# Kernel optimization log

Hardware: AMD Instinct MI355X
Metric: run time of the kernel (lower is better)

The kernel has to match this reference:

```python
import jax, jax.numpy as jnp
import numpy as np

EPS_NORM = 1e-8  # F.normalize eps (clamps norm from below)
EPS_ERR = 1e-8   # eps added under sqrt for the error


def _normalize(x, eps=EPS_NORM):
    n = jnp.linalg.norm(x, axis=-1, keepdims=True)
    return x / jnp.maximum(n, eps)


def _frame_basis(frames):
    """frames: [b, n, 3, 3]; points a, b, c are the COLUMNS (unbind dim=-1).
    Returns origin b_pt [b, n, 3] and orthonormal basis E [b, n, 3(basis k), 3(xyz d)]."""
    a, b_pt, c = frames[..., 0], frames[..., 1], frames[..., 2]
    w1 = _normalize(a - b_pt)
    w2 = _normalize(c - b_pt)
    e1 = _normalize(w1 + w2)
    e2 = _normalize(w2 - w1)
    e3 = jnp.cross(e1, e2)
    return b_pt, jnp.stack([e1, e2, e3], axis=-2)


def _pair_transform(coords, frames):
    """t[b,i,j,k] = dot(coords[b,i] - origin[b,j], E[b,j,k]).
    Exploits linearity to avoid materializing the [b,n,n,3] difference tensor."""
    origin, E = _frame_basis(frames)
    proj_c = jnp.einsum('bid,bjkd->bijk', coords, E)          # [b,n,n,3]
    proj_o = jnp.einsum('bjd,bjkd->bjk', origin, E)           # [b,n,3]
    return proj_c - proj_o[:, None, :, :]


def setup_inputs() -> dict:
    key = jax.random.key(0)
    k1, k2, k3, k4 = jax.random.split(key, 4)
    b, n = 2, 2048
    return {
        'pred_coords': jax.random.normal(k1, (b, n, 3), dtype=jnp.float32),
        'true_coords': jax.random.normal(k2, (b, n, 3), dtype=jnp.float32),
        'pred_frames': jax.random.normal(k3, (b, n, 3, 3), dtype=jnp.float32),
        'true_frames': jax.random.normal(k4, (b, n, 3, 3), dtype=jnp.float32),
    }


def reference(pred_coords, true_coords, pred_frames, true_frames):
    # coord index i is expressed in frame index j -> errors [b, n, n]
    t_pred = _pair_transform(pred_coords, pred_frames)
    t_true = _pair_transform(true_coords, true_frames)
    diff = t_pred - t_true
    return jnp.sqrt(jnp.sum(diff * diff, axis=-1) + EPS_ERR)
```

## Files before the change

kernel.cpp:

```cpp
#include <hip/hip_runtime.h>
#include <math.h>

#define EPS_NORM 1e-8f
#define EPS_ERR  1e-8f

__device__ inline void norm3(float& x, float& y, float& z) {
    float nn = sqrtf(x*x + y*y + z*z);
    float inv = 1.0f / fmaxf(nn, EPS_NORM);
    x *= inv; y *= inv; z *= inv;
}

__device__ inline void basis_from_frame(const float* __restrict__ F, size_t base,
                                        float* e , float* o ) {
    float ax = F[base + 0], bx = F[base + 1], cx = F[base + 2];
    float ay = F[base + 3], by = F[base + 4], cy = F[base + 5];
    float az = F[base + 6], bz = F[base + 7], cz = F[base + 8];
    float w1x = ax - bx, w1y = ay - by, w1z = az - bz;
    float w2x = cx - bx, w2y = cy - by, w2z = cz - bz;
    norm3(w1x, w1y, w1z);
    norm3(w2x, w2y, w2z);
    float e1x = w1x + w2x, e1y = w1y + w2y, e1z = w1z + w2z;
    float e2x = w2x - w1x, e2y = w2y - w1y, e2z = w2z - w1z;
    norm3(e1x, e1y, e1z);
    norm3(e2x, e2y, e2z);
    float e3x = e1y * e2z - e1z * e2y;
    float e3y = e1z * e2x - e1x * e2z;
    float e3z = e1x * e2y - e1y * e2x;
    e[0] = e1x; e[1] = e1y; e[2] = e1z;
    e[3] = e2x; e[4] = e2y; e[5] = e2z;
    e[6] = e3x; e[7] = e3y; e[8] = e3z;
    o[0] = bx * e1x + by * e1y + bz * e1z;
    o[1] = bx * e2x + by * e2y + bz * e2z;
    o[2] = bx * e3x + by * e3y + bz * e3z;
}

__global__ __launch_bounds__(256) void frames_kernel(
    const float* __restrict__ predF, const float* __restrict__ trueF,
    float* __restrict__ fd, int total_bn)
{
    int idx = blockIdx.x * 256 + threadIdx.x;
    if (idx >= total_bn) return;
    float ep[9], op[3], et[9], ot[3];
    basis_from_frame(predF, (size_t)idx * 9, ep, op);
    basis_from_frame(trueF, (size_t)idx * 9, et, ot);
    #pragma unroll
    for (int k = 0; k < 9; ++k) fd[(size_t)k * total_bn + idx] = ep[k];
    #pragma unroll
    for (int k = 0; k < 9; ++k) fd[(size_t)(9 + k) * total_bn + idx] = et[k];
    #pragma unroll
    for (int k = 0; k < 3; ++k) fd[(size_t)(18 + k) * total_bn + idx] = op[k] - ot[k];
}

template<int IT>
__global__ __launch_bounds__(256) void pair_err_kernel(
    const float* __restrict__ cp, const float* __restrict__ ct,
    const float* __restrict__ fd, float* __restrict__ out, int n, int total_bn)
{
    int j  = blockIdx.x * 256 + threadIdx.x;
    int bi = blockIdx.z;
    if (j >= n) return;
    int idx = bi * n + j;

    float f[21];
    #pragma unroll
    for (int c = 0; c < 21; ++c) f[c] = fd[(size_t)c * total_bn + idx];

    const int i0 = blockIdx.y * IT;
    const int iters = min(IT, n - i0);
    size_t obase = ((size_t)bi * n + i0) * n + j;
    size_t cbase = ((size_t)bi * n + i0) * 3;

    #pragma unroll 8
    for (int ii = 0; ii < iters; ++ii) {
        float px = cp[cbase + ii * 3 + 0], py = cp[cbase + ii * 3 + 1], pz = cp[cbase + ii * 3 + 2];
        float tx = ct[cbase + ii * 3 + 0], ty = ct[cbase + ii * 3 + 1], tz = ct[cbase + ii * 3 + 2];
        float d0 = px * f[0] + py * f[1] + pz * f[2] - (tx * f[ 9] + ty * f[10] + tz * f[11]) - f[18];
        float d1 = px * f[3] + py * f[4] + pz * f[5] - (tx * f[12] + ty * f[13] + tz * f[14]) - f[19];
        float d2 = px * f[6] + py * f[7] + pz * f[8] - (tx * f[15] + ty * f[16] + tz * f[17]) - f[20];
        out[obase + (size_t)ii * n] = sqrtf(d0 * d0 + d1 * d1 + d2 * d2 + EPS_ERR);
    }
}

extern "C" void kernel_launch(void* const* d_in, const int* in_sizes, int n_in,
                              void* d_out, int out_size, void* d_ws, size_t ws_size,
                              hipStream_t stream) {
    const float* pred_coords = (const float*)d_in[0];
    const float* true_coords = (const float*)d_in[1];
    const float* pred_frames = (const float*)d_in[2];
    const float* true_frames = (const float*)d_in[3];
    float* out = (float*)d_out;

    int total_bn = in_sizes[0] / 3;
    int n = (int)((long long)out_size / total_bn);
    int b = total_bn / n;

    float* fd = (float*)d_ws;

    int blocks1 = (total_bn + 255) / 256;
    frames_kernel<<<blocks1, 256, 0, stream>>>(pred_frames, true_frames, fd, total_bn);

    constexpr int IT = 32;
    dim3 grid((n + 255) / 256, (n + IT - 1) / IT, b);
    pair_err_kernel<IT><<<grid, 256, 0, stream>>>(pred_coords, true_coords, fd, out, n, total_bn);
}
```

Measured before the change: 84.08 us.

## Fuse frame basis computation into pair kernel and store two columns per thread

Drops the separate frames kernel and its workspace round-trip. Each pair-error block now recomputes the orthonormal bases for its own j columns straight from the raw frame inputs. Each thread handles two adjacent j columns and writes them as a float2 store, halving the coordinate loads per output. The cost is redundant basis recomputation in every i-tile block (n/32 times per frame), more registers, and uncoalesced 9-float frame loads.

```diff
diff --git a/kernel.cpp b/kernel.cpp
--- a/kernel.cpp
+++ b/kernel.cpp
@@ -34,50 +34,84 @@
     o[2] = bx * e3x + by * e3y + bz * e3z;
 }
 
-__global__ __launch_bounds__(256) void frames_kernel(
-    const float* __restrict__ predF, const float* __restrict__ trueF,
-    float* __restrict__ fd, int total_bn)
-{
-    int idx = blockIdx.x * 256 + threadIdx.x;
-    if (idx >= total_bn) return;
-    float ep[9], op[3], et[9], ot[3];
-    basis_from_frame(predF, (size_t)idx * 9, ep, op);
-    basis_from_frame(trueF, (size_t)idx * 9, et, ot);
+__device__ inline void frame21(const float* __restrict__ pF, const float* __restrict__ tF,
+                               size_t base, float* f) {
+    float e[9], o[3], e2[9], o2[3];
+    basis_from_frame(pF, base, e, o);
+    basis_from_frame(tF, base, e2, o2);
     #pragma unroll
-    for (int k = 0; k < 9; ++k) fd[(size_t)k * total_bn + idx] = ep[k];
+    for (int k = 0; k < 9; ++k) f[k] = e[k];
     #pragma unroll
-    for (int k = 0; k < 9; ++k) fd[(size_t)(9 + k) * total_bn + idx] = et[k];
+    for (int k = 0; k < 9; ++k) f[9 + k] = e2[k];
     #pragma unroll
-    for (int k = 0; k < 3; ++k) fd[(size_t)(18 + k) * total_bn + idx] = op[k] - ot[k];
+    for (int k = 0; k < 3; ++k) f[18 + k] = o[k] - o2[k];
+}
+
+__device__ inline float perr(const float* f, float px, float py, float pz,
+                             float tx, float ty, float tz) {
+    float d0 = px * f[0] + py * f[1] + pz * f[2] - (tx * f[ 9] + ty * f[10] + tz * f[11]) - f[18];
+    float d1 = px * f[3] + py * f[4] + pz * f[5] - (tx * f[12] + ty * f[13] + tz * f[14]) - f[19];
+    float d2 = px * f[6] + py * f[7] + pz * f[8] - (tx * f[15] + ty * f[16] + tz * f[17]) - f[20];
+    return sqrtf(d0 * d0 + d1 * d1 + d2 * d2 + EPS_ERR);
 }
 
 template<int IT>
-__global__ __launch_bounds__(256) void pair_err_kernel(
+__global__ __launch_bounds__(256) void fused2_kernel(
     const float* __restrict__ cp, const float* __restrict__ ct,
-    const float* __restrict__ fd, float* __restrict__ out, int n, int total_bn)
+    const float* __restrict__ pF, const float* __restrict__ tF,
+    float* __restrict__ out, int n)
 {
-    int j  = blockIdx.x * 256 + threadIdx.x;
-    int bi = blockIdx.z;
-    if (j >= n) return;
-    int idx = bi * n + j;
+    const int bi = blockIdx.z;
+    const int j0 = (blockIdx.x * 256 + threadIdx.x) * 2;
+    if (j0 >= n) return;
 
-    float f[21];
-    #pragma unroll
-    for (int c = 0; c < 21; ++c) f[c] = fd[(size_t)c * total_bn + idx];
+    float fa[21], fb[21];
+    frame21(pF, tF, ((size_t)bi * n + j0) * 9, fa);
+    frame21(pF, tF, ((size_t)bi * n + j0 + 1) * 9, fb);
 
     const int i0 = blockIdx.y * IT;
     const int iters = min(IT, n - i0);
-    size_t obase = ((size_t)bi * n + i0) * n + j;
-    size_t cbase = ((size_t)bi * n + i0) * 3;
+    const float* cpb = cp + ((size_t)bi * n + i0) * 3;
+    const float* ctb = ct + ((size_t)bi * n + i0) * 3;
+    float* ob = out + ((size_t)bi * n + i0) * n + j0;
 
-    #pragma unroll 8
+    #pragma unroll 4
     for (int ii = 0; ii < iters; ++ii) {
-        float px = cp[cbase + ii * 3 + 0], py = cp[cbase + ii * 3 + 1], pz = cp[cbase + ii * 3 + 2];
-        float tx = ct[cbase + ii * 3 + 0], ty = ct[cbase + ii * 3 + 1], tz = ct[cbase + ii * 3 + 2];
-        float d0 = px * f[0] + py * f[1] + pz * f[2] - (tx * f[ 9] + ty * f[10] + tz * f[11]) - f[18];
-        float d1 = px * f[3] + py * f[4] + pz * f[5] - (tx * f[12] + ty * f[13] + tz * f[14]) - f[19];
-        float d2 = px * f[6] + py * f[7] + pz * f[8] - (tx * f[15] + ty * f[16] + tz * f[17]) - f[20];
-        out[obase + (size_t)ii * n] = sqrtf(d0 * d0 + d1 * d1 + d2 * d2 + EPS_ERR);
+        float px = cpb[ii * 3 + 0], py = cpb[ii * 3 + 1], pz = cpb[ii * 3 + 2];
+        float tx = ctb[ii * 3 + 0], ty = ctb[ii * 3 + 1], tz = ctb[ii * 3 + 2];
+        float2 r;
+        r.x = perr(fa, px, py, pz, tx, ty, tz);
+        r.y = perr(fb, px, py, pz, tx, ty, tz);
+        *reinterpret_cast<float2*>(ob) = r;
+        ob += n;
+    }
+}
+
+template<int IT>
+__global__ __launch_bounds__(256) void fused1_kernel(
+    const float* __restrict__ cp, const float* __restrict__ ct,
+    const float* __restrict__ pF, const float* __restrict__ tF,
+    float* __restrict__ out, int n)
+{
+    const int bi = blockIdx.z;
+    const int j = blockIdx.x * 256 + threadIdx.x;
+    if (j >= n) return;
+
+    float fa[21];
+    frame21(pF, tF, ((size_t)bi * n + j) * 9, fa);
+
+    const int i0 = blockIdx.y * IT;
+    const int iters = min(IT, n - i0);
+    const float* cpb = cp + ((size_t)bi * n + i0) * 3;
+    const float* ctb = ct + ((size_t)bi * n + i0) * 3;
+    float* ob = out + ((size_t)bi * n + i0) * n + j;
+
+    #pragma unroll 4
+    for (int ii = 0; ii < iters; ++ii) {
+        float px = cpb[ii * 3 + 0], py = cpb[ii * 3 + 1], pz = cpb[ii * 3 + 2];
+        float tx = ctb[ii * 3 + 0], ty = ctb[ii * 3 + 1], tz = ctb[ii * 3 + 2];
+        *ob = perr(fa, px, py, pz, tx, ty, tz);
+        ob += n;
     }
 }
 
@@ -94,12 +128,15 @@
     int n = (int)((long long)out_size / total_bn);
     int b = total_bn / n;
 
-    float* fd = (float*)d_ws;
-
-    int blocks1 = (total_bn + 255) / 256;
-    frames_kernel<<<blocks1, 256, 0, stream>>>(pred_frames, true_frames, fd, total_bn);
-
     constexpr int IT = 32;
-    dim3 grid((n + 255) / 256, (n + IT - 1) / IT, b);
-    pair_err_kernel<IT><<<grid, 256, 0, stream>>>(pred_coords, true_coords, fd, out, n, total_bn);
+    if ((n & 1) == 0) {
+        int jthreads = n / 2;
+        dim3 grid((jthreads + 255) / 256, (n + IT - 1) / IT, b);
+        fused2_kernel<IT><<<grid, 256, 0, stream>>>(pred_coords, true_coords,
+                                                    pred_frames, true_frames, out, n);
+    } else {
+        dim3 grid((n + 255) / 256, (n + IT - 1) / IT, b);
+        fused1_kernel<IT><<<grid, 256, 0, stream>>>(pred_coords, true_coords,
+                                                    pred_frames, true_frames, out, n);
+    }
 }
```

Result: faster. 81.33 us (-3.3%).
